# Kernel tuning notes

Hardware: AMD Instinct MI355X
Metric: run time of the kernel (lower is better)

Reference implementation:

```python
import jax, jax.numpy as jnp
import numpy as np

B = 16            # batch of graphs
N = 512           # n_node
D = 32            # embedding_dim
MAXN = 16         # max_neighbors
E = MAXN * (N - 1)   # 8176 edges per graph
SLEFT = N * D
FSS = 601         # full_support_size
NA = N - 1        # num_actions (so one-hot rows == B*n_node)
IN0 = D + 1       # sa feature dim
NTOT = B * N


def _gat(x, snd, rcv, W, a_src, a_dst, b):
    # single-head GATConv, add_self_loops=False
    h = x @ W                                            # [BN, C]
    e = (h * a_src).sum(-1)[snd] + (h * a_dst).sum(-1)[rcv]
    e = jnp.where(e > 0, e, 0.2 * e)                     # LeakyReLU(0.2)
    m = jax.ops.segment_max(e, rcv, num_segments=NTOT)   # segment softmax
    m = jnp.where(jnp.isfinite(m), m, 0.0)
    ee = jnp.exp(e - m[rcv])
    den = jax.ops.segment_sum(ee, rcv, num_segments=NTOT)
    alpha = ee / (den[rcv] + 1e-16)
    return jax.ops.segment_sum(alpha[:, None] * h[snd], rcv, num_segments=NTOT) + b


def _ln(x, s, o):
    # hk.LayerNorm(axis=-2): normalize over node axis, scale/offset over features
    x3 = x.reshape(B, N, -1)
    mu = x3.mean(axis=1, keepdims=True)
    var = ((x3 - mu) ** 2).mean(axis=1, keepdims=True)
    return ((x3 - mu) * jax.lax.rsqrt(var + 1e-5) * s + o).reshape(B * N, -1)


def _gat_params(key, din, dout):
    k1, k2, k3 = jax.random.split(key, 3)
    sc = 1.0 / np.sqrt(din)
    return (jax.random.normal(k1, (din, dout), jnp.float32) * sc,
            jax.random.normal(k2, (dout,), jnp.float32) * sc,
            jax.random.normal(k3, (dout,), jnp.float32) * sc,
            jnp.zeros((dout,), jnp.float32))


def setup_inputs():
    key = jax.random.key(0)
    ks = jax.random.split(key, 4)
    nodes = jax.random.normal(ks[0], (B, SLEFT), jnp.float32)
    snd = jax.random.randint(ks[1], (B, E), 0, N).astype(jnp.float32)
    rcv = jax.random.randint(ks[2], (B, E), 0, N).astype(jnp.float32)
    ns = jnp.concatenate([nodes, snd, rcv], axis=1)      # [B, SLEFT + 2E]
    a = jax.random.randint(ks[3], (B,), 0, NA + 1)
    inp = {"ns": ns, "a": a}
    dims = [(IN0, 4 * D), (4 * D, 2 * D), (2 * D, 2 * D), (2 * D, D)]
    rdims = [(IN0, FSS), (FSS, FSS), (FSS, FSS), (FSS, FSS)]
    for i, (di, do) in enumerate(dims, 1):
        W, asrc, adst, b = _gat_params(jax.random.fold_in(key, 100 + i), di, do)
        inp.update({f"W{i}": W, f"a{i}s": asrc, f"a{i}d": adst, f"b{i}": b})
        if i < 4:
            inp.update({f"s{i}": jnp.ones((do,), jnp.float32), f"o{i}": jnp.zeros((do,), jnp.float32)})
    for i, (di, do) in enumerate(rdims, 1):
        W, asrc, adst, b = _gat_params(jax.random.fold_in(key, 200 + i), di, do)
        inp.update({f"rW{i}": W, f"ra{i}s": asrc, f"ra{i}d": adst, f"rb{i}": b})
        if i < 4:
            inp.update({f"rs{i}": jnp.ones((FSS,), jnp.float32), f"ro{i}": jnp.zeros((FSS,), jnp.float32)})
    return inp


def reference(ns, a,
              W1, a1s, a1d, b1, s1, o1,
              W2, a2s, a2d, b2, s2, o2,
              W3, a3s, a3d, b3, s3, o3,
              W4, a4s, a4d, b4,
              rW1, ra1s, ra1d, rb1, rs1, ro1,
              rW2, ra2s, ra2d, rb2, rs2, ro2,
              rW3, ra3s, ra3d, rb3, rs3, ro3,
              rW4, ra4s, ra4d, rb4):
    # gbatch: offset per-graph indices into one big graph
    off = (jnp.arange(B, dtype=jnp.int32) * N)[:, None]
    snd = (ns[:, SLEFT:SLEFT + E].astype(jnp.int32) + off).reshape(-1)
    rcv = (ns[:, SLEFT + E:SLEFT + 2 * E].astype(jnp.int32) + off).reshape(-1)
    nodes = ns[:, :SLEFT].reshape(B * N, D)
    sa = jnp.concatenate([nodes, jax.nn.one_hot(a, NA + 1).reshape(-1, 1)], axis=1)
    # reward head
    r = jax.nn.relu(_ln(_gat(sa, snd, rcv, rW1, ra1s, ra1d, rb1), rs1, ro1))
    r = jax.nn.relu(_ln(_gat(r, snd, rcv, rW2, ra2s, ra2d, rb2), rs2, ro2))
    r = jax.nn.relu(_ln(_gat(r, snd, rcv, rW3, ra3s, ra3d, rb3), rs3, ro3))
    r = _gat(r, snd, rcv, rW4, ra4s, ra4d, rb4).reshape(B, N, FSS).sum(axis=1)
    # next-state head
    f = jax.nn.relu(_ln(_gat(sa, snd, rcv, W1, a1s, a1d, b1), s1, o1))
    f = jax.nn.relu(_ln(_gat(f, snd, rcv, W2, a2s, a2d, b2), s2, o2))
    f = jax.nn.relu(_ln(_gat(f, snd, rcv, W3, a3s, a3d, b3), s3, o3))
    f = _gat(f, snd, rcv, W4, a4s, a4d, b4).reshape(B, N * D)
    ns_new = jnp.concatenate([f, ns[:, SLEFT:]], axis=1)
    return (r, ns_new)
```

## Files before the change

### kernel.cpp

```cpp
#include <hip/hip_runtime.h>
#include <math.h>

#define B_ 16
#define N_ 512
#define D_ 32
#define E_ 8176
#define SLEFT_ 16384
#define FSS_ 601
#define BN_ (B_*N_)
#define BE_ (B_*E_)
#define NSROW_ (SLEFT_ + 2*E_)
#define OUT_R_ (B_*FSS_)
#define HLD_ 768

typedef __attribute__((ext_vector_type(8))) short short8;
typedef __attribute__((ext_vector_type(4))) float f32x4;

typedef __attribute__((address_space(3))) uint lds_uint;
typedef __attribute__((address_space(1))) const uint g_uint;

__device__ __forceinline__ void gl_lds16(const ushort* gp, ushort* lp) {
  __builtin_amdgcn_global_load_lds((g_uint*)gp, (lds_uint*)lp, 16, 0, 0);
}

__device__ __forceinline__ ushort f2b(float f) {
  uint u = __builtin_bit_cast(uint, f);
  u += 0x7FFFu + ((u >> 16) & 1u);
  return (ushort)(u >> 16);
}
__device__ __forceinline__ float b2f(ushort h) {
  return __builtin_bit_cast(float, ((uint)h) << 16);
}


__global__ __launch_bounds__(256) void k_indices(const float* __restrict__ ns,
                                                 int* __restrict__ src_i,
                                                 int* __restrict__ dst_i,
                                                 int* __restrict__ cnt) {
  int idx = blockIdx.x*256 + threadIdx.x;
  if (idx >= BE_) return;
  int b = idx / E_;
  int j = idx - b*E_;
  const float* row = ns + (size_t)b*NSROW_;
  int s = (int)row[SLEFT_ + j];
  int r = (int)row[SLEFT_ + E_ + j];
  src_i[idx] = b*N_ + s;
  int dst = b*N_ + r;
  dst_i[idx] = dst;
  atomicAdd(&cnt[dst], 1);
}

__global__ __launch_bounds__(1024) void k_scan(const int* __restrict__ cnt,
                                               int* __restrict__ rowptr) {
  __shared__ int part[1024];
  int t = threadIdx.x;
  int base = t*8;
  int loc[8]; int s = 0;
  #pragma unroll
  for (int i=0;i<8;i++){ loc[i]=cnt[base+i]; s+=loc[i]; }
  part[t]=s; __syncthreads();
  for (int off=1; off<1024; off<<=1) {
    int v = (t>=off)?part[t-off]:0;
    __syncthreads();
    part[t]+=v;
    __syncthreads();
  }
  int ex = (t==0)?0:part[t-1];
  #pragma unroll
  for (int i=0;i<8;i++){ rowptr[base+i]=ex; ex+=loc[i]; }
  if (t==1023) rowptr[BN_]=ex;
}

__global__ __launch_bounds__(256) void k_scatter(const int* __restrict__ src_i,
                                                 const int* __restrict__ dst_i,
                                                 const int* __restrict__ rowptr,
                                                 int* __restrict__ fill,
                                                 int* __restrict__ csr_src) {
  int idx = blockIdx.x*256+threadIdx.x;
  if (idx>=BE_) return;
  int dst = dst_i[idx];
  int pos = rowptr[dst] + atomicAdd(&fill[dst],1);
  csr_src[pos] = src_i[idx];
}


__global__ __launch_bounds__(256) void k_sa(const float* __restrict__ ns,
                                            const int* __restrict__ a,
                                            ushort* __restrict__ sa) {
  int idx = blockIdx.x*256+threadIdx.x;
  if (idx >= BN_*64) return;
  int v = idx >> 6, c = idx & 63;
  int b = v >> 9, n = v & 511;
  float val = 0.f;
  if (c < 32)       val = ns[(size_t)b*NSROW_ + n*32 + c];
  else if (c == 32) val = (a[b]==n) ? 1.f : 0.f;
  sa[idx] = f2b(val);
}


struct WtP { const float* Wr[4]; const float* Wn[4]; ushort* T[4]; };

__global__ __launch_bounds__(256) void k_wt_tr(WtP p) {
  int t = blockIdx.x;
  int s, base, KP, DINR, DINN, DOUTN, KOFF;
  if (t < 48)        { s=0; base=0;    KP=64;  DINR=33;  DINN=33;  DOUTN=128; KOFF=0;   }
  else if (t < 600)  { s=1; base=48;   KP=736; DINR=601; DINN=128; DOUTN=64;  KOFF=608; }
  else if (t < 1104) { s=2; base=600;  KP=672; DINR=601; DINN=64;  DOUTN=64;  KOFF=608; }
  else               { s=3; base=1104; KP=672; DINR=601; DINN=64;  DOUTN=32;  KOFF=608; }
  int ti = t - base;
  int kt = ti / 24, nt = ti - kt*24;
  int k0 = kt*32, n0 = nt*32;
  __shared__ float tile[32][33];
  int tid = threadIdx.x;
  int cc = tid & 31, rr = tid >> 5;
  #pragma unroll
  for (int it=0; it<4; it++) {
    int k = k0 + it*8 + rr;
    int n = n0 + cc;
    float v = 0.f;
    if (n < 640) { if (n < 601 && k < DINR) v = p.Wr[s][(size_t)k*601 + n]; }
    else { int nn = n-640, kk = k-KOFF;
           if (nn < DOUTN && kk >= 0 && kk < DINN) v = p.Wn[s][(size_t)kk*DOUTN + nn]; }
    tile[it*8+rr][cc] = v;
  }
  __syncthreads();
  #pragma unroll
  for (int it=0; it<4; it++) {
    int n = n0 + it*8 + rr;
    int k = k0 + cc;
    p.T[s][(size_t)n*KP + k] = f2b(tile[cc][it*8+rr]);
  }
}


__global__ __launch_bounds__(256) void k_gemm(const ushort* __restrict__ A,
                                              const ushort* __restrict__ Bt,
                                              ushort* __restrict__ C,
                                              float* __restrict__ esed,
                                              const float* __restrict__ asr,
                                              const float* __restrict__ adr,
                                              const float* __restrict__ asn,
                                              const float* __restrict__ adn,
                                              int Kpad, int dn) {
  __shared__ ushort Asm[64*32];
  __shared__ ushort Bsm[128*32];
  int tid = threadIdx.x;
  int rowBase = blockIdx.y * 64;
  int colBase = blockIdx.x * 128;
  int wave = tid >> 6, lane = tid & 63;
  int wr = (wave >> 1) * 32, wc = (wave & 1) * 64;
  int lm = lane & 15, lk = (lane >> 4) * 8;

  f32x4 acc[2][4];
  #pragma unroll
  for (int i=0;i<2;i++)
    #pragma unroll
    for (int j=0;j<4;j++) acc[i][j] = (f32x4){0.f,0.f,0.f,0.f};

  int t0 = tid, t1 = tid + 256;
  const ushort* Ag0 = A  + (size_t)(rowBase + (t0>>2))*Kpad + (t0&3)*8;
  const ushort* Bg0 = Bt + (size_t)(colBase + (t0>>2))*Kpad + (t0&3)*8;
  const ushort* Bg1 = Bt + (size_t)(colBase + (t1>>2))*Kpad + (t1&3)*8;
  ushort* Al0 = &Asm[t0*8];
  ushort* Bl0 = &Bsm[t0*8];
  ushort* Bl1 = &Bsm[t1*8];

  for (int k0 = 0; k0 < Kpad; k0 += 32) {
    gl_lds16(Ag0 + k0, Al0);
    gl_lds16(Bg0 + k0, Bl0);
    gl_lds16(Bg1 + k0, Bl1);
    __syncthreads();
    short8 af[2], bfr[4];
    #pragma unroll
    for (int i=0;i<2;i++) af[i]  = *(short8*)&Asm[(wr + i*16 + lm)*32 + lk];
    #pragma unroll
    for (int j=0;j<4;j++) bfr[j] = *(short8*)&Bsm[(wc + j*16 + lm)*32 + lk];
    #pragma unroll
    for (int i=0;i<2;i++)
      #pragma unroll
      for (int j=0;j<4;j++)
        acc[i][j] = __builtin_amdgcn_mfma_f32_16x16x32_bf16(af[i], bfr[j], acc[i][j], 0,0,0);
    __syncthreads();
  }

  float asv[4], adv[4];
  #pragma unroll
  for (int j=0;j<4;j++) {
    int col = colBase + wc + j*16 + lm;
    float s = 0.f, d = 0.f;
    if (col < 601)      { s = asr[col];     d = adr[col]; }
    else if (col >= 640 && col - 640 < dn) { s = asn[col-640]; d = adn[col-640]; }
    asv[j] = s; adv[j] = d;
  }
  int cr = lane >> 4;
  int ct2 = blockIdx.x*2 + (wc >> 6);
  #pragma unroll
  for (int i=0;i<2;i++) {
    #pragma unroll
    for (int j=0;j<4;j++) {
      int col = colBase + wc + j*16 + lm;
      #pragma unroll
      for (int g=0; g<4; g++) {
        int row = rowBase + wr + i*16 + cr*4 + g;
        C[(size_t)row*HLD_ + col] = f2b(acc[i][j][g]);
      }
    }
    #pragma unroll
    for (int g=0; g<4; g++) {
      float se = 0.f, sd = 0.f;
      #pragma unroll
      for (int j=0;j<4;j++) { se += acc[i][j][g]*asv[j]; sd += acc[i][j][g]*adv[j]; }
      #pragma unroll
      for (int o=1;o<16;o<<=1) { se += __shfl_xor(se,o,64); sd += __shfl_xor(sd,o,64); }
      if (lm == 0) {
        int row = rowBase + wr + i*16 + cr*4 + g;
        esed[(size_t)row*24 + ct2*2 + 0] = se;
        esed[(size_t)row*24 + ct2*2 + 1] = sd;
      }
    }
  }
}


__global__ __launch_bounds__(256) void k_agg(const ushort* __restrict__ h,
                                             const float* __restrict__ esed,
                                             const int* __restrict__ rowptr,
                                             const int* __restrict__ csr,
                                             const float* __restrict__ bias_r,
                                             const float* __restrict__ bias_n,
                                             ushort* __restrict__ g,
                                             int dn) {
  int wid = threadIdx.x>>6, lane = threadIdx.x&63;
  int bid = blockIdx.x;
  int xcd = bid & 7, slot = bid >> 3;
  int graph = xcd + ((slot >> 7) << 3);
  int v = graph*512 + (slot & 127)*4 + wid;
  int s0 = rowptr[v], e0 = rowptr[v+1];
  int deg = e0 - s0;

  float edr = 0.f, edn = 0.f;
  {
    const float* ep = esed + (size_t)v*24;
    #pragma unroll
    for (int t=0;t<10;t++) edr += ep[2*t+1];
    edn = ep[21] + ep[23];
  }

  int ch0 = lane, ch1 = lane + 64;
  bool a1 = ch1 < 96;
  float acc0[8], acc1[8];
  #pragma unroll
  for (int q=0;q<8;q++){ acc0[q]=0.f; acc1[q]=0.f; }

  if (deg <= 64) {
    bool has = lane < deg;
    int u = 0; float er = -__builtin_inff(), en = -__builtin_inff();
    if (has) {
      u = csr[s0 + lane];
      const float* ep = esed + (size_t)u*24;
      float sr = 0.f;
      #pragma unroll
      for (int t=0;t<10;t++) sr += ep[2*t];
      float sn = ep[20] + ep[22];
      er = sr + edr; er = er > 0.f ? er : 0.2f*er;
      en = sn + edn; en = en > 0.f ? en : 0.2f*en;
    }
    float mr = er, mn = en;
    #pragma unroll
    for (int o=32;o;o>>=1) { mr = fmaxf(mr, __shfl_xor(mr,o,64)); mn = fmaxf(mn, __shfl_xor(mn,o,64)); }
    float pr = has ? __expf(er - mr) : 0.f;
    float pn = has ? __expf(en - mn) : 0.f;
    float dr = pr, dnm = pn;
    #pragma unroll
    for (int o=32;o;o>>=1) { dr += __shfl_xor(dr,o,64); dnm += __shfl_xor(dnm,o,64); }
    pr *= 1.f/(dr + 1e-16f);
    pn *= 1.f/(dnm + 1e-16f);

    short8 A0{}, Bv0{}, A1{}, Bv1{};
    float w0r=0.f, w0n=0.f, w1r=0.f, w1n=0.f;
    if (deg > 0) {
      w0r = __shfl(pr, 0, 64); w0n = __shfl(pn, 0, 64); int uu = __shfl(u, 0, 64);
      const ushort* hp = h + (size_t)uu*HLD_;
      A0 = *(const short8*)&hp[ch0*8];
      if (a1) Bv0 = *(const short8*)&hp[ch1*8];
    }
    if (deg > 1) {
      w1r = __shfl(pr, 1, 64); w1n = __shfl(pn, 1, 64); int uu = __shfl(u, 1, 64);
      const ushort* hp = h + (size_t)uu*HLD_;
      A1 = *(const short8*)&hp[ch0*8];
      if (a1) Bv1 = *(const short8*)&hp[ch1*8];
    }
    bool c1r = ch1 < 80;
    for (int t = 0; t < deg; ++t) {
      short8 A2{}, Bv2{}; float w2r=0.f, w2n=0.f;
      if (t+2 < deg) {
        w2r = __shfl(pr, t+2, 64); w2n = __shfl(pn, t+2, 64); int uu = __shfl(u, t+2, 64);
        const ushort* hp = h + (size_t)uu*HLD_;
        A2 = *(const short8*)&hp[ch0*8];
        if (a1) Bv2 = *(const short8*)&hp[ch1*8];
      }
      #pragma unroll
      for (int q=0;q<8;q++) acc0[q] += w0r * b2f((ushort)A0[q]);
      if (a1) {
        float w = c1r ? w0r : w0n;
        #pragma unroll
        for (int q=0;q<8;q++) acc1[q] += w * b2f((ushort)Bv0[q]);
      }
      A0=A1; Bv0=Bv1; w0r=w1r; w0n=w1n;
      A1=A2; Bv1=Bv2; w1r=w2r; w1n=w2n;
    }
  } else {
    float mr = -__builtin_inff(), mn = -__builtin_inff();
    for (int j = s0 + lane; j < e0; j += 64) {
      const float* ep = esed + (size_t)csr[j]*24;
      float sr=0.f; for (int t=0;t<10;t++) sr += ep[2*t];
      float sn = ep[20]+ep[22];
      float er = sr + edr; er = er>0.f?er:0.2f*er;
      float en = sn + edn; en = en>0.f?en:0.2f*en;
      mr = fmaxf(mr, er); mn = fmaxf(mn, en);
    }
    #pragma unroll
    for (int o=32;o;o>>=1) { mr=fmaxf(mr,__shfl_xor(mr,o,64)); mn=fmaxf(mn,__shfl_xor(mn,o,64)); }
    float dr=0.f, dnm=0.f;
    for (int j = s0 + lane; j < e0; j += 64) {
      const float* ep = esed + (size_t)csr[j]*24;
      float sr=0.f; for (int t=0;t<10;t++) sr += ep[2*t];
      float sn = ep[20]+ep[22];
      float er = sr + edr; er = er>0.f?er:0.2f*er;
      float en = sn + edn; en = en>0.f?en:0.2f*en;
      dr += __expf(er-mr); dnm += __expf(en-mn);
    }
    #pragma unroll
    for (int o=32;o;o>>=1) { dr+=__shfl_xor(dr,o,64); dnm+=__shfl_xor(dnm,o,64); }
    float ir = 1.f/(dr+1e-16f), in_ = 1.f/(dnm+1e-16f);
    bool c1r = ch1 < 80;
    for (int j = s0; j < e0; ++j) {
      int uu = csr[j];
      const float* ep = esed + (size_t)uu*24;
      float sr=0.f; for (int t=0;t<10;t++) sr += ep[2*t];
      float sn = ep[20]+ep[22];
      float er = sr + edr; er = er>0.f?er:0.2f*er;
      float en = sn + edn; en = en>0.f?en:0.2f*en;
      float wr2 = __expf(er-mr)*ir, wn2 = __expf(en-mn)*in_;
      const ushort* hp = h + (size_t)uu*HLD_;
      short8 hv = *(const short8*)&hp[ch0*8];
      #pragma unroll
      for (int q=0;q<8;q++) acc0[q] += wr2 * b2f((ushort)hv[q]);
      if (a1) {
        short8 hv2 = *(const short8*)&hp[ch1*8];
        float w = c1r ? wr2 : wn2;
        #pragma unroll
        for (int q=0;q<8;q++) acc1[q] += w * b2f((ushort)hv2[q]);
      }
    }
  }

  ushort* gv = g + (size_t)v*HLD_;
  {
    int cb = ch0*8;
    short8 ov;
    #pragma unroll
    for (int q=0;q<8;q++) ov[q] = (short)f2b(acc0[q] + bias_r[cb+q]);
    *(short8*)&gv[cb] = ov;
  }
  if (a1) {
    int cb = ch1*8;
    short8 ov;
    #pragma unroll
    for (int q=0;q<8;q++) {
      int c = cb+q;
      float val;
      if (c < 601)                         val = acc1[q] + bias_r[c];
      else if (c >= 640 && (c-640) < dn)   val = acc1[q] + bias_n[c-640];
      else                                 val = 0.f;
      ov[q] = (short)f2b(val);
    }
    *(short8*)&gv[cb] = ov;
  }
}


__global__ __launch_bounds__(256) void k_ln_stats(const ushort* __restrict__ g,
                                                  float* __restrict__ st) {
  int b = blockIdx.y, z = blockIdx.z; int n0 = z*64;
  int lc = threadIdx.x & 63, r0 = threadIdx.x >> 6;
  int c = blockIdx.x*64 + lc;
  float s=0.f, q=0.f;
  #pragma unroll 4
  for (int i=0;i<16;i++) {
    int n = n0 + r0*16 + i;
    float x = b2f(g[(size_t)(b*N_+n)*HLD_ + c]);
    s+=x; q+=x*x;
  }
  __shared__ float S[4][64], Q[4][64];
  S[r0][lc]=s; Q[r0][lc]=q; __syncthreads();
  if (r0==0) {
    st[((size_t)(z*2+0)*B_ + b)*HLD_ + c] = S[0][lc]+S[1][lc]+S[2][lc]+S[3][lc];
    st[((size_t)(z*2+1)*B_ + b)*HLD_ + c] = Q[0][lc]+Q[1][lc]+Q[2][lc]+Q[3][lc];
  }
}


__global__ __launch_bounds__(256) void k_ln_apply(const ushort* __restrict__ g,
                                                  const float* __restrict__ st,
                                                  const float* __restrict__ scr,
                                                  const float* __restrict__ ofr,
                                                  const float* __restrict__ scn,
                                                  const float* __restrict__ ofn,
                                                  ushort* __restrict__ xb,
                                                  int dn, int Kpad) {
  int tid = threadIdx.x;
  int pp = blockIdx.x*128 + (tid & 127);
  int c0 = pp*2;
  if (c0 >= Kpad) return;
  int vbase = blockIdx.y*16;
  int b = vbase >> 9;
  float mv[2], av[2];
  #pragma unroll
  for (int q=0;q<2;q++) {
    int c = c0+q;
    int cs; bool valid; float scale, offs;
    if (c < 608) { cs = c; valid = c < 601;
                   scale = valid ? scr[c] : 0.f; offs = valid ? ofr[c] : 0.f; }
    else { int cn = c - 608; cs = 640 + cn; valid = cn < dn;
           scale = valid ? scn[cn] : 0.f; offs = valid ? ofn[cn] : 0.f; }
    float mul = 0.f, add = 0.f;
    if (valid) {
      float s=0.f, qq=0.f;
      #pragma unroll
      for (int z=0;z<8;z++) {
        s  += st[((size_t)(z*2+0)*B_ + b)*HLD_ + cs];
        qq += st[((size_t)(z*2+1)*B_ + b)*HLD_ + cs];
      }
      float mu = s*(1.f/N_);
      float var = qq*(1.f/N_) - mu*mu;
      float rs = rsqrtf(var+1e-5f);
      mul = rs*scale;
      add = offs - mu*rs*scale;
    }
    mv[q] = mul; av[q] = add;
  }
  int cs0 = (c0 < 608) ? c0 : 640 + (c0 - 608);
  for (int i = tid >> 7; i < 16; i += 2) {
    int v = vbase + i;
    uint gg = *(const uint*)&g[(size_t)v*HLD_ + cs0];
    float x0 = b2f((ushort)(gg & 0xFFFFu));
    float x1 = b2f((ushort)(gg >> 16));
    float y0 = x0*mv[0] + av[0]; y0 = y0 > 0.f ? y0 : 0.f;
    float y1 = x1*mv[1] + av[1]; y1 = y1 > 0.f ? y1 : 0.f;
    *(uint*)&xb[(size_t)v*Kpad + c0] = ((uint)f2b(y1) << 16) | f2b(y0);
  }
}


__global__ __launch_bounds__(256) void k_rsum(const ushort* __restrict__ g,
                                              float* __restrict__ rsp) {
  int b = blockIdx.y, z = blockIdx.z; int n0 = z*64;
  int lc = threadIdx.x & 63, r0 = threadIdx.x>>6;
  int c = blockIdx.x*64 + lc;
  float s = 0.f;
  if (c < FSS_) {
    #pragma unroll 4
    for (int i=0;i<16;i++) {
      int n = n0 + r0*16 + i;
      s += b2f(g[(size_t)(b*N_+n)*HLD_ + c]);
    }
  }
  __shared__ float S[4][64];
  S[r0][lc]=s; __syncthreads();
  if (r0==0 && c<FSS_)
    rsp[((size_t)z*B_ + b)*FSS_ + c] = S[0][lc]+S[1][lc]+S[2][lc]+S[3][lc];
}


__global__ __launch_bounds__(256) void k_final(const float* __restrict__ rsp,
                                               const ushort* __restrict__ g,
                                               const float* __restrict__ ns,
                                               float* __restrict__ out) {
  int idx = blockIdx.x*256+threadIdx.x;
  if (idx < OUT_R_) {
    int b = idx / FSS_, c = idx - b*FSS_;
    float s = 0.f;
    #pragma unroll
    for (int z=0;z<8;z++) s += rsp[((size_t)z*B_ + b)*FSS_ + c];
    out[idx] = s;
  } else {
    int j2 = idx - OUT_R_;
    if (j2 >= B_*NSROW_) return;
    int b = j2 / NSROW_; int j = j2 - b*NSROW_;
    float v;
    if (j < SLEFT_) {
      int n = j >> 5, c = j & 31;
      v = b2f(g[(size_t)(b*N_+n)*HLD_ + 640 + c]);
    } else {
      v = ns[(size_t)b*NSROW_ + j];
    }
    out[idx] = v;
  }
}


extern "C" void kernel_launch(void* const* d_in, const int* in_sizes, int n_in,
                              void* d_out, int out_size, void* d_ws, size_t ws_size,
                              hipStream_t stream) {
  const float* ns = (const float*)d_in[0];
  const int*   a  = (const int*)d_in[1];

  const float *W[4], *As[4], *Ad[4], *Bb[4], *Sc[3], *Of[3];
  const float *rW[4], *rAs[4], *rAd[4], *rBb[4], *rSc[3], *rOf[3];
  int p = 2;
  for (int i=0;i<4;i++){
    W[i]=(const float*)d_in[p++]; As[i]=(const float*)d_in[p++];
    Ad[i]=(const float*)d_in[p++]; Bb[i]=(const float*)d_in[p++];
    if (i<3){ Sc[i]=(const float*)d_in[p++]; Of[i]=(const float*)d_in[p++]; }
  }
  for (int i=0;i<4;i++){
    rW[i]=(const float*)d_in[p++]; rAs[i]=(const float*)d_in[p++];
    rAd[i]=(const float*)d_in[p++]; rBb[i]=(const float*)d_in[p++];
    if (i<3){ rSc[i]=(const float*)d_in[p++]; rOf[i]=(const float*)d_in[p++]; }
  }

  char* w = (char*)d_ws;
  auto carve = [&](size_t bytes)->void* {
    void* r = (void*)w;
    w += (bytes + 255) & ~(size_t)255;
    return r;
  };
  ushort* xb   = (ushort*)carve((size_t)BN_*736*2);
  ushort* hbuf = (ushort*)carve((size_t)BN_*HLD_*2);
  ushort* gbuf = (ushort*)carve((size_t)BN_*HLD_*2);
  ushort* sabf = (ushort*)carve((size_t)BN_*64*2);
  float* esed  = (float*)carve((size_t)BN_*24*4);
  float* stp   = (float*)carve((size_t)16*B_*HLD_*4);
  float* rsp   = (float*)carve((size_t)8*B_*FSS_*4);
  int* src_i   = (int*)carve((size_t)BE_*4);
  int* dst_i   = (int*)carve((size_t)BE_*4);
  int* cnt     = (int*)carve((size_t)2*BN_*4);
  int* fill    = cnt + BN_;
  int* rowptr  = (int*)carve((size_t)(BN_+1)*4);
  int* csr_src = (int*)carve((size_t)BE_*4);
  ushort* Wt[4];
  Wt[0] = (ushort*)carve((size_t)768*64*2);
  Wt[1] = (ushort*)carve((size_t)768*736*2);
  Wt[2] = (ushort*)carve((size_t)768*672*2);
  Wt[3] = (ushort*)carve((size_t)768*672*2);

  float* out = (float*)d_out;

  hipMemsetAsync(cnt, 0, (size_t)2*BN_*4, stream);

  k_indices<<<(BE_+255)/256, 256, 0, stream>>>(ns, src_i, dst_i, cnt);
  k_scan<<<1, 1024, 0, stream>>>(cnt, rowptr);
  k_scatter<<<(BE_+255)/256, 256, 0, stream>>>(src_i, dst_i, rowptr, fill, csr_src);
  k_sa<<<(BN_*64+255)/256, 256, 0, stream>>>(ns, a, sabf);

  WtP wtp;
  for (int i=0;i<4;i++){ wtp.Wr[i]=rW[i]; wtp.Wn[i]=W[i]; wtp.T[i]=Wt[i]; }
  k_wt_tr<<<1608, 256, 0, stream>>>(wtp);

  dim3 ggrid(6, BN_/64);

  k_gemm<<<ggrid, 256, 0, stream>>>(sabf, Wt[0], hbuf, esed, rAs[0],rAd[0],As[0],Ad[0], 64, 128);
  k_agg<<<BN_/4, 256, 0, stream>>>(hbuf, esed, rowptr, csr_src, rBb[0], Bb[0], gbuf, 128);
  k_ln_stats<<<dim3(12, B_, 8), 256, 0, stream>>>(gbuf, stp);
  k_ln_apply<<<dim3(3, BN_/16), 256, 0, stream>>>(gbuf, stp, rSc[0],rOf[0],Sc[0],Of[0], xb, 128, 736);

  k_gemm<<<ggrid, 256, 0, stream>>>(xb, Wt[1], hbuf, esed, rAs[1],rAd[1],As[1],Ad[1], 736, 64);
  k_agg<<<BN_/4, 256, 0, stream>>>(hbuf, esed, rowptr, csr_src, rBb[1], Bb[1], gbuf, 64);
  k_ln_stats<<<dim3(12, B_, 8), 256, 0, stream>>>(gbuf, stp);
  k_ln_apply<<<dim3(3, BN_/16), 256, 0, stream>>>(gbuf, stp, rSc[1],rOf[1],Sc[1],Of[1], xb, 64, 672);

  k_gemm<<<ggrid, 256, 0, stream>>>(xb, Wt[2], hbuf, esed, rAs[2],rAd[2],As[2],Ad[2], 672, 64);
  k_agg<<<BN_/4, 256, 0, stream>>>(hbuf, esed, rowptr, csr_src, rBb[2], Bb[2], gbuf, 64);
  k_ln_stats<<<dim3(12, B_, 8), 256, 0, stream>>>(gbuf, stp);
  k_ln_apply<<<dim3(3, BN_/16), 256, 0, stream>>>(gbuf, stp, rSc[2],rOf[2],Sc[2],Of[2], xb, 64, 672);

  k_gemm<<<ggrid, 256, 0, stream>>>(xb, Wt[3], hbuf, esed, rAs[3],rAd[3],As[3],Ad[3], 672, 32);
  k_agg<<<BN_/4, 256, 0, stream>>>(hbuf, esed, rowptr, csr_src, rBb[3], Bb[3], gbuf, 32);

  k_rsum<<<dim3(10, B_, 8), 256, 0, stream>>>(gbuf, rsp);
  k_final<<<(OUT_R_ + B_*NSROW_ + 255)/256, 256, 0, stream>>>(rsp, gbuf, ns, out);
}
```

Before: 409.6 us.

## Split GAT aggregation into edge-weight pass and LDS-tiled per-graph aggregation with fused stats

The GEMM epilogue now reduces attention logits into four compact per-node arrays with atomics, replacing the 24-wide partial layout. A new k_ew kernel computes normalized softmax edge weights once per edge. A new k_aggt kernel stages a graph's 64-column slice of h in LDS and aggregates from there, and it also computes the per-graph column sums and sums of squares. This removes the separate LayerNorm-stats and reward-sum kernels. The trade-offs are only 192 blocks with a serial 128-node loop per wave, a 64 KB LDS footprint, scalar per-column LDS reads, atomic contention, and an extra memset per layer.

```diff
diff --git a/kernel.cpp b/kernel.cpp
--- a/kernel.cpp
+++ b/kernel.cpp
@@ -194,6 +194,7 @@
   }
   int cr = lane >> 4;
   int ct2 = blockIdx.x*2 + (wc >> 6);
+  float* esp = (ct2 < 10) ? esed : esed + 2*BN_;
   #pragma unroll
   for (int i=0;i<2;i++) {
     #pragma unroll
@@ -214,189 +215,154 @@
       for (int o=1;o<16;o<<=1) { se += __shfl_xor(se,o,64); sd += __shfl_xor(sd,o,64); }
       if (lm == 0) {
         int row = rowBase + wr + i*16 + cr*4 + g;
-        esed[(size_t)row*24 + ct2*2 + 0] = se;
-        esed[(size_t)row*24 + ct2*2 + 1] = sd;
+        atomicAdd(&esp[row], se);
+        atomicAdd(&esp[BN_ + row], sd);
       }
     }
   }
 }
 
 
-__global__ __launch_bounds__(256) void k_agg(const ushort* __restrict__ h,
-                                             const float* __restrict__ esed,
-                                             const int* __restrict__ rowptr,
-                                             const int* __restrict__ csr,
-                                             const float* __restrict__ bias_r,
-                                             const float* __restrict__ bias_n,
-                                             ushort* __restrict__ g,
-                                             int dn) {
+__global__ __launch_bounds__(256) void k_ew(const float* __restrict__ esed,
+                                            const int* __restrict__ rowptr,
+                                            const int* __restrict__ csr,
+                                            float* __restrict__ wrv,
+                                            float* __restrict__ wnv) {
+  const float* es_r = esed;
+  const float* ed_r = esed + BN_;
+  const float* es_n = esed + 2*BN_;
+  const float* ed_n = esed + 3*BN_;
   int wid = threadIdx.x>>6, lane = threadIdx.x&63;
-  int bid = blockIdx.x;
-  int xcd = bid & 7, slot = bid >> 3;
-  int graph = xcd + ((slot >> 7) << 3);
-  int v = graph*512 + (slot & 127)*4 + wid;
+  int v = blockIdx.x*4 + wid;
   int s0 = rowptr[v], e0 = rowptr[v+1];
   int deg = e0 - s0;
-
-  float edr = 0.f, edn = 0.f;
-  {
-    const float* ep = esed + (size_t)v*24;
-    #pragma unroll
-    for (int t=0;t<10;t++) edr += ep[2*t+1];
-    edn = ep[21] + ep[23];
-  }
-
-  int ch0 = lane, ch1 = lane + 64;
-  bool a1 = ch1 < 96;
-  float acc0[8], acc1[8];
-  #pragma unroll
-  for (int q=0;q<8;q++){ acc0[q]=0.f; acc1[q]=0.f; }
+  if (deg == 0) return;
+  float edr = ed_r[v], edn = ed_n[v];
 
   if (deg <= 64) {
     bool has = lane < deg;
-    int u = 0; float er = -__builtin_inff(), en = -__builtin_inff();
+    float er = -__builtin_inff(), en = -__builtin_inff();
     if (has) {
-      u = csr[s0 + lane];
-      const float* ep = esed + (size_t)u*24;
-      float sr = 0.f;
-      #pragma unroll
-      for (int t=0;t<10;t++) sr += ep[2*t];
-      float sn = ep[20] + ep[22];
-      er = sr + edr; er = er > 0.f ? er : 0.2f*er;
-      en = sn + edn; en = en > 0.f ? en : 0.2f*en;
+      int u = csr[s0 + lane];
+      er = es_r[u] + edr; er = er > 0.f ? er : 0.2f*er;
+      en = es_n[u] + edn; en = en > 0.f ? en : 0.2f*en;
     }
     float mr = er, mn = en;
     #pragma unroll
     for (int o=32;o;o>>=1) { mr = fmaxf(mr, __shfl_xor(mr,o,64)); mn = fmaxf(mn, __shfl_xor(mn,o,64)); }
     float pr = has ? __expf(er - mr) : 0.f;
     float pn = has ? __expf(en - mn) : 0.f;
-    float dr = pr, dnm = pn;
-    #pragma unroll
-    for (int o=32;o;o>>=1) { dr += __shfl_xor(dr,o,64); dnm += __shfl_xor(dnm,o,64); }
-    pr *= 1.f/(dr + 1e-16f);
-    pn *= 1.f/(dnm + 1e-16f);
-
-    short8 A0{}, Bv0{}, A1{}, Bv1{};
-    float w0r=0.f, w0n=0.f, w1r=0.f, w1n=0.f;
-    if (deg > 0) {
-      w0r = __shfl(pr, 0, 64); w0n = __shfl(pn, 0, 64); int uu = __shfl(u, 0, 64);
-      const ushort* hp = h + (size_t)uu*HLD_;
-      A0 = *(const short8*)&hp[ch0*8];
-      if (a1) Bv0 = *(const short8*)&hp[ch1*8];
-    }
-    if (deg > 1) {
-      w1r = __shfl(pr, 1, 64); w1n = __shfl(pn, 1, 64); int uu = __shfl(u, 1, 64);
-      const ushort* hp = h + (size_t)uu*HLD_;
-      A1 = *(const short8*)&hp[ch0*8];
-      if (a1) Bv1 = *(const short8*)&hp[ch1*8];
-    }
-    bool c1r = ch1 < 80;
-    for (int t = 0; t < deg; ++t) {
-      short8 A2{}, Bv2{}; float w2r=0.f, w2n=0.f;
-      if (t+2 < deg) {
-        w2r = __shfl(pr, t+2, 64); w2n = __shfl(pn, t+2, 64); int uu = __shfl(u, t+2, 64);
-        const ushort* hp = h + (size_t)uu*HLD_;
-        A2 = *(const short8*)&hp[ch0*8];
-        if (a1) Bv2 = *(const short8*)&hp[ch1*8];
-      }
-      #pragma unroll
-      for (int q=0;q<8;q++) acc0[q] += w0r * b2f((ushort)A0[q]);
-      if (a1) {
-        float w = c1r ? w0r : w0n;
-        #pragma unroll
-        for (int q=0;q<8;q++) acc1[q] += w * b2f((ushort)Bv0[q]);
-      }
-      A0=A1; Bv0=Bv1; w0r=w1r; w0n=w1n;
-      A1=A2; Bv1=Bv2; w1r=w2r; w1n=w2n;
+    float dr = pr, dn2 = pn;
+    #pragma unroll
+    for (int o=32;o;o>>=1) { dr += __shfl_xor(dr,o,64); dn2 += __shfl_xor(dn2,o,64); }
+    if (has) {
+      wrv[s0 + lane] = pr * (1.f/(dr + 1e-16f));
+      wnv[s0 + lane] = pn * (1.f/(dn2 + 1e-16f));
     }
   } else {
     float mr = -__builtin_inff(), mn = -__builtin_inff();
     for (int j = s0 + lane; j < e0; j += 64) {
-      const float* ep = esed + (size_t)csr[j]*24;
-      float sr=0.f; for (int t=0;t<10;t++) sr += ep[2*t];
-      float sn = ep[20]+ep[22];
-      float er = sr + edr; er = er>0.f?er:0.2f*er;
-      float en = sn + edn; en = en>0.f?en:0.2f*en;
+      int u = csr[j];
+      float er = es_r[u] + edr; er = er>0.f?er:0.2f*er;
+      float en = es_n[u] + edn; en = en>0.f?en:0.2f*en;
       mr = fmaxf(mr, er); mn = fmaxf(mn, en);
     }
     #pragma unroll
     for (int o=32;o;o>>=1) { mr=fmaxf(mr,__shfl_xor(mr,o,64)); mn=fmaxf(mn,__shfl_xor(mn,o,64)); }
-    float dr=0.f, dnm=0.f;
+    float dr=0.f, dn2=0.f;
     for (int j = s0 + lane; j < e0; j += 64) {
-      const float* ep = esed + (size_t)csr[j]*24;
-      float sr=0.f; for (int t=0;t<10;t++) sr += ep[2*t];
-      float sn = ep[20]+ep[22];
-      float er = sr + edr; er = er>0.f?er:0.2f*er;
-      float en = sn + edn; en = en>0.f?en:0.2f*en;
-      dr += __expf(er-mr); dnm += __expf(en-mn);
-    }
-    #pragma unroll
-    for (int o=32;o;o>>=1) { dr+=__shfl_xor(dr,o,64); dnm+=__shfl_xor(dnm,o,64); }
-    float ir = 1.f/(dr+1e-16f), in_ = 1.f/(dnm+1e-16f);
-    bool c1r = ch1 < 80;
-    for (int j = s0; j < e0; ++j) {
-      int uu = csr[j];
-      const float* ep = esed + (size_t)uu*24;
-      float sr=0.f; for (int t=0;t<10;t++) sr += ep[2*t];
-      float sn = ep[20]+ep[22];
-      float er = sr + edr; er = er>0.f?er:0.2f*er;
-      float en = sn + edn; en = en>0.f?en:0.2f*en;
-      float wr2 = __expf(er-mr)*ir, wn2 = __expf(en-mn)*in_;
-      const ushort* hp = h + (size_t)uu*HLD_;
-      short8 hv = *(const short8*)&hp[ch0*8];
-      #pragma unroll
-      for (int q=0;q<8;q++) acc0[q] += wr2 * b2f((ushort)hv[q]);
-      if (a1) {
-        short8 hv2 = *(const short8*)&hp[ch1*8];
-        float w = c1r ? wr2 : wn2;
-        #pragma unroll
-        for (int q=0;q<8;q++) acc1[q] += w * b2f((ushort)hv2[q]);
+      int u = csr[j];
+      float er = es_r[u] + edr; er = er>0.f?er:0.2f*er;
+      float en = es_n[u] + edn; en = en>0.f?en:0.2f*en;
+      dr += __expf(er-mr); dn2 += __expf(en-mn);
+    }
+    #pragma unroll
+    for (int o=32;o;o>>=1) { dr+=__shfl_xor(dr,o,64); dn2+=__shfl_xor(dn2,o,64); }
+    float ir = 1.f/(dr+1e-16f), in_ = 1.f/(dn2+1e-16f);
+    for (int j = s0 + lane; j < e0; j += 64) {
+      int u = csr[j];
+      float er = es_r[u] + edr; er = er>0.f?er:0.2f*er;
+      float en = es_n[u] + edn; en = en>0.f?en:0.2f*en;
+      wrv[j] = __expf(er-mr)*ir;
+      wnv[j] = __expf(en-mn)*in_;
+    }
+  }
+}
+
+
+__global__ __launch_bounds__(256) void k_aggt(const ushort* __restrict__ h,
+                                              const float* __restrict__ wrv,
+                                              const float* __restrict__ wnv,
+                                              const int* __restrict__ rowptr,
+                                              const int* __restrict__ csr,
+                                              const float* __restrict__ bias_r,
+                                              const float* __restrict__ bias_n,
+                                              ushort* __restrict__ g,
+                                              float* __restrict__ st,
+                                              int dn) {
+  __shared__ ushort Hl[512*64];
+  int bid = blockIdx.x;
+  int graph = bid & 15;
+  int chunk = bid >> 4;
+  int c0 = chunk * 64;
+  const float* wv = (chunk < 10) ? wrv : wnv;
+  int lane = threadIdx.x & 63, wid = threadIdx.x >> 6;
+
+  {
+    int t = threadIdx.x;
+    int col8 = (t & 7) * 8;
+    int rb = t >> 3;
+    #pragma unroll
+    for (int i = 0; i < 16; i++) {
+      int r = i*32 + rb;
+      *(short8*)&Hl[r*64 + col8] =
+        *(const short8*)&h[(size_t)(graph*512 + r)*HLD_ + c0 + col8];
+    }
+  }
+  __syncthreads();
+
+  int col = c0 + lane;
+  bool valid; float bv;
+  if (col < 601)                         { bv = bias_r[col];     valid = true; }
+  else if (col >= 640 && col - 640 < dn) { bv = bias_n[col-640]; valid = true; }
+  else                                   { bv = 0.f;             valid = false; }
+
+  float ssum = 0.f, sq = 0.f;
+  for (int i = 0; i < 128; i++) {
+    int vn = graph*512 + wid*128 + i;
+    int s0 = rowptr[vn], e0 = rowptr[vn+1];
+    float acc = 0.f;
+    for (int base = s0; base < e0; base += 64) {
+      int j = base + lane;
+      float wj = 0.f; int uj = 0;
+      if (j < e0) { wj = wv[j]; uj = csr[j] & 511; }
+      int cl = e0 - base; if (cl > 64) cl = 64;
+      float wb0 = __shfl(wj, 0, 64); int ub0 = __shfl(uj, 0, 64);
+      ushort hv0 = Hl[ub0*64 + lane];
+      for (int t = 0; t < cl; ++t) {
+        float wb1 = 0.f; int ub1 = 0; ushort hv1 = 0;
+        if (t+1 < cl) {
+          wb1 = __shfl(wj, t+1, 64); ub1 = __shfl(uj, t+1, 64);
+          hv1 = Hl[ub1*64 + lane];
+        }
+        acc += wb0 * b2f(hv0);
+        wb0 = wb1; hv0 = hv1;
       }
     }
-  }
-
-  ushort* gv = g + (size_t)v*HLD_;
-  {
-    int cb = ch0*8;
-    short8 ov;
-    #pragma unroll
-    for (int q=0;q<8;q++) ov[q] = (short)f2b(acc0[q] + bias_r[cb+q]);
-    *(short8*)&gv[cb] = ov;
-  }
-  if (a1) {
-    int cb = ch1*8;
-    short8 ov;
-    #pragma unroll
-    for (int q=0;q<8;q++) {
-      int c = cb+q;
-      float val;
-      if (c < 601)                         val = acc1[q] + bias_r[c];
-      else if (c >= 640 && (c-640) < dn)   val = acc1[q] + bias_n[c-640];
-      else                                 val = 0.f;
-      ov[q] = (short)f2b(val);
-    }
-    *(short8*)&gv[cb] = ov;
-  }
-}
-
-
-__global__ __launch_bounds__(256) void k_ln_stats(const ushort* __restrict__ g,
-                                                  float* __restrict__ st) {
-  int b = blockIdx.y, z = blockIdx.z; int n0 = z*64;
-  int lc = threadIdx.x & 63, r0 = threadIdx.x >> 6;
-  int c = blockIdx.x*64 + lc;
-  float s=0.f, q=0.f;
-  #pragma unroll 4
-  for (int i=0;i<16;i++) {
-    int n = n0 + r0*16 + i;
-    float x = b2f(g[(size_t)(b*N_+n)*HLD_ + c]);
-    s+=x; q+=x*x;
-  }
-  __shared__ float S[4][64], Q[4][64];
-  S[r0][lc]=s; Q[r0][lc]=q; __syncthreads();
-  if (r0==0) {
-    st[((size_t)(z*2+0)*B_ + b)*HLD_ + c] = S[0][lc]+S[1][lc]+S[2][lc]+S[3][lc];
-    st[((size_t)(z*2+1)*B_ + b)*HLD_ + c] = Q[0][lc]+Q[1][lc]+Q[2][lc]+Q[3][lc];
+    float val = valid ? acc + bv : 0.f;
+    g[(size_t)vn*HLD_ + col] = f2b(val);
+    ssum += val; sq += val*val;
+  }
+  __syncthreads();
+  float* Sf = (float*)Hl;
+  Sf[wid*64 + lane]       = ssum;
+  Sf[256 + wid*64 + lane] = sq;
+  __syncthreads();
+  if (wid == 0) {
+    float s = Sf[lane] + Sf[64+lane] + Sf[128+lane] + Sf[192+lane];
+    float q = Sf[256+lane] + Sf[320+lane] + Sf[384+lane] + Sf[448+lane];
+    st[(size_t)graph*HLD_ + col]        = s;
+    st[(size_t)(B_+graph)*HLD_ + col]   = q;
   }
 }
 
@@ -426,12 +392,8 @@
            scale = valid ? scn[cn] : 0.f; offs = valid ? ofn[cn] : 0.f; }
     float mul = 0.f, add = 0.f;
     if (valid) {
-      float s=0.f, qq=0.f;
-      #pragma unroll
-      for (int z=0;z<8;z++) {
-        s  += st[((size_t)(z*2+0)*B_ + b)*HLD_ + cs];
-        qq += st[((size_t)(z*2+1)*B_ + b)*HLD_ + cs];
-      }
+      float s  = st[(size_t)b*HLD_ + cs];
+      float qq = st[(size_t)(B_+b)*HLD_ + cs];
       float mu = s*(1.f/N_);
       float var = qq*(1.f/N_) - mu*mu;
       float rs = rsqrtf(var+1e-5f);
@@ -453,37 +415,14 @@
 }
 
 
-__global__ __launch_bounds__(256) void k_rsum(const ushort* __restrict__ g,
-                                              float* __restrict__ rsp) {
-  int b = blockIdx.y, z = blockIdx.z; int n0 = z*64;
-  int lc = threadIdx.x & 63, r0 = threadIdx.x>>6;
-  int c = blockIdx.x*64 + lc;
-  float s = 0.f;
-  if (c < FSS_) {
-    #pragma unroll 4
-    for (int i=0;i<16;i++) {
-      int n = n0 + r0*16 + i;
-      s += b2f(g[(size_t)(b*N_+n)*HLD_ + c]);
-    }
-  }
-  __shared__ float S[4][64];
-  S[r0][lc]=s; __syncthreads();
-  if (r0==0 && c<FSS_)
-    rsp[((size_t)z*B_ + b)*FSS_ + c] = S[0][lc]+S[1][lc]+S[2][lc]+S[3][lc];
-}
-
-
-__global__ __launch_bounds__(256) void k_final(const float* __restrict__ rsp,
+__global__ __launch_bounds__(256) void k_final(const float* __restrict__ st,
                                                const ushort* __restrict__ g,
                                                const float* __restrict__ ns,
                                                float* __restrict__ out) {
   int idx = blockIdx.x*256+threadIdx.x;
   if (idx < OUT_R_) {
     int b = idx / FSS_, c = idx - b*FSS_;
-    float s = 0.f;
-    #pragma unroll
-    for (int z=0;z<8;z++) s += rsp[((size_t)z*B_ + b)*FSS_ + c];
-    out[idx] = s;
+    out[idx] = st[(size_t)b*HLD_ + c];
   } else {
     int j2 = idx - OUT_R_;
     if (j2 >= B_*NSROW_) return;
@@ -530,9 +469,10 @@
   ushort* hbuf = (ushort*)carve((size_t)BN_*HLD_*2);
   ushort* gbuf = (ushort*)carve((size_t)BN_*HLD_*2);
   ushort* sabf = (ushort*)carve((size_t)BN_*64*2);
-  float* esed  = (float*)carve((size_t)BN_*24*4);
-  float* stp   = (float*)carve((size_t)16*B_*HLD_*4);
-  float* rsp   = (float*)carve((size_t)8*B_*FSS_*4);
+  float* esed  = (float*)carve((size_t)4*BN_*4);
+  float* wrv   = (float*)carve((size_t)BE_*4);
+  float* wnv   = (float*)carve((size_t)BE_*4);
+  float* st    = (float*)carve((size_t)2*B_*HLD_*4);
   int* src_i   = (int*)carve((size_t)BE_*4);
   int* dst_i   = (int*)carve((size_t)BE_*4);
   int* cnt     = (int*)carve((size_t)2*BN_*4);
@@ -560,24 +500,23 @@
 
   dim3 ggrid(6, BN_/64);
 
-  k_gemm<<<ggrid, 256, 0, stream>>>(sabf, Wt[0], hbuf, esed, rAs[0],rAd[0],As[0],Ad[0], 64, 128);
-  k_agg<<<BN_/4, 256, 0, stream>>>(hbuf, esed, rowptr, csr_src, rBb[0], Bb[0], gbuf, 128);
-  k_ln_stats<<<dim3(12, B_, 8), 256, 0, stream>>>(gbuf, stp);
-  k_ln_apply<<<dim3(3, BN_/16), 256, 0, stream>>>(gbuf, stp, rSc[0],rOf[0],Sc[0],Of[0], xb, 128, 736);
-
-  k_gemm<<<ggrid, 256, 0, stream>>>(xb, Wt[1], hbuf, esed, rAs[1],rAd[1],As[1],Ad[1], 736, 64);
-  k_agg<<<BN_/4, 256, 0, stream>>>(hbuf, esed, rowptr, csr_src, rBb[1], Bb[1], gbuf, 64);
-  k_ln_stats<<<dim3(12, B_, 8), 256, 0, stream>>>(gbuf, stp);
-  k_ln_apply<<<dim3(3, BN_/16), 256, 0, stream>>>(gbuf, stp, rSc[1],rOf[1],Sc[1],Of[1], xb, 64, 672);
-
-  k_gemm<<<ggrid, 256, 0, stream>>>(xb, Wt[2], hbuf, esed, rAs[2],rAd[2],As[2],Ad[2], 672, 64);
-  k_agg<<<BN_/4, 256, 0, stream>>>(hbuf, esed, rowptr, csr_src, rBb[2], Bb[2], gbuf, 64);
-  k_ln_stats<<<dim3(12, B_, 8), 256, 0, stream>>>(gbuf, stp);
-  k_ln_apply<<<dim3(3, BN_/16), 256, 0, stream>>>(gbuf, stp, rSc[2],rOf[2],Sc[2],Of[2], xb, 64, 672);
-
-  k_gemm<<<ggrid, 256, 0, stream>>>(xb, Wt[3], hbuf, esed, rAs[3],rAd[3],As[3],Ad[3], 672, 32);
-  k_agg<<<BN_/4, 256, 0, stream>>>(hbuf, esed, rowptr, csr_src, rBb[3], Bb[3], gbuf, 32);
-
-  k_rsum<<<dim3(10, B_, 8), 256, 0, stream>>>(gbuf, rsp);
-  k_final<<<(OUT_R_ + B_*NSROW_ + 255)/256, 256, 0, stream>>>(rsp, gbuf, ns, out);
-}
+  const ushort* xin[4] = { sabf, xb, xb, xb };
+  int Kp[4]  = { 64, 736, 672, 672 };
+  int dns[4] = { 128, 64, 64, 32 };
+
+  for (int L=0; L<4; ++L) {
+    hipMemsetAsync(esed, 0, (size_t)4*BN_*4, stream);
+    k_gemm<<<ggrid, 256, 0, stream>>>(xin[L], Wt[L], hbuf, esed,
+                                      rAs[L], rAd[L], As[L], Ad[L], Kp[L], dns[L]);
+    k_ew<<<BN_/4, 256, 0, stream>>>(esed, rowptr, csr_src, wrv, wnv);
+    k_aggt<<<192, 256, 0, stream>>>(hbuf, wrv, wnv, rowptr, csr_src,
+                                    rBb[L], Bb[L], gbuf, st, dns[L]);
+    if (L < 3) {
+      int Kpn = (L==0) ? 736 : 672;
+      k_ln_apply<<<dim3(3, BN_/16), 256, 0, stream>>>(gbuf, st,
+                  rSc[L], rOf[L], Sc[L], Of[L], xb, dns[L], Kpn);
+    }
+  }
+
+  k_final<<<(OUT_R_ + B_*NSROW_ + 255)/256, 256, 0, stream>>>(st, gbuf, ns, out);
+}
```

Result: slower. 1.400 ms (+241.9%).

## Reduce attention logits with atomics into compact arrays and batch neighbor gathers

Applied to the files above, without the earlier changes.

The GEMM epilogue now atomically accumulates per-node source and destination attention scores into four compact BN-length arrays, replacing the 24-float partial-sum row per node. This lets the aggregation kernel read one float per neighbor instead of summing twelve strided partials, at the cost of a memset before each layer and float atomics whose summation order is nondeterministic. The neighbor gather loop is also changed from a two-deep software-pipelined prefetch to batches of four loads issued before the accumulation, and the layer launches are folded into a loop.

```diff
diff --git a/kernel.cpp b/kernel.cpp
--- a/kernel.cpp
+++ b/kernel.cpp
@@ -194,6 +194,7 @@
   }
   int cr = lane >> 4;
   int ct2 = blockIdx.x*2 + (wc >> 6);
+  float* esp = (ct2 < 10) ? esed : esed + 2*BN_;
   #pragma unroll
   for (int i=0;i<2;i++) {
     #pragma unroll
@@ -214,8 +215,8 @@
       for (int o=1;o<16;o<<=1) { se += __shfl_xor(se,o,64); sd += __shfl_xor(sd,o,64); }
       if (lm == 0) {
         int row = rowBase + wr + i*16 + cr*4 + g;
-        esed[(size_t)row*24 + ct2*2 + 0] = se;
-        esed[(size_t)row*24 + ct2*2 + 1] = sd;
+        atomicAdd(&esp[row], se);
+        atomicAdd(&esp[BN_ + row], sd);
       }
     }
   }
@@ -230,6 +231,10 @@
                                              const float* __restrict__ bias_n,
                                              ushort* __restrict__ g,
                                              int dn) {
+  const float* es_r = esed;
+  const float* ed_r = esed + BN_;
+  const float* es_n = esed + 2*BN_;
+  const float* ed_n = esed + 3*BN_;
   int wid = threadIdx.x>>6, lane = threadIdx.x&63;
   int bid = blockIdx.x;
   int xcd = bid & 7, slot = bid >> 3;
@@ -237,17 +242,11 @@
   int v = graph*512 + (slot & 127)*4 + wid;
   int s0 = rowptr[v], e0 = rowptr[v+1];
   int deg = e0 - s0;
-
-  float edr = 0.f, edn = 0.f;
-  {
-    const float* ep = esed + (size_t)v*24;
-    #pragma unroll
-    for (int t=0;t<10;t++) edr += ep[2*t+1];
-    edn = ep[21] + ep[23];
-  }
+  float edr = ed_r[v], edn = ed_n[v];
 
   int ch0 = lane, ch1 = lane + 64;
   bool a1 = ch1 < 96;
+  bool c1r = ch1 < 80;
   float acc0[8], acc1[8];
   #pragma unroll
   for (int q=0;q<8;q++){ acc0[q]=0.f; acc1[q]=0.f; }
@@ -257,13 +256,8 @@
     int u = 0; float er = -__builtin_inff(), en = -__builtin_inff();
     if (has) {
       u = csr[s0 + lane];
-      const float* ep = esed + (size_t)u*24;
-      float sr = 0.f;
-      #pragma unroll
-      for (int t=0;t<10;t++) sr += ep[2*t];
-      float sn = ep[20] + ep[22];
-      er = sr + edr; er = er > 0.f ? er : 0.2f*er;
-      en = sn + edn; en = en > 0.f ? en : 0.2f*en;
+      er = es_r[u] + edr; er = er > 0.f ? er : 0.2f*er;
+      en = es_n[u] + edn; en = en > 0.f ? en : 0.2f*en;
     }
     float mr = er, mn = en;
     #pragma unroll
@@ -276,71 +270,58 @@
     pr *= 1.f/(dr + 1e-16f);
     pn *= 1.f/(dnm + 1e-16f);
 
-    short8 A0{}, Bv0{}, A1{}, Bv1{};
-    float w0r=0.f, w0n=0.f, w1r=0.f, w1n=0.f;
-    if (deg > 0) {
-      w0r = __shfl(pr, 0, 64); w0n = __shfl(pn, 0, 64); int uu = __shfl(u, 0, 64);
-      const ushort* hp = h + (size_t)uu*HLD_;
-      A0 = *(const short8*)&hp[ch0*8];
-      if (a1) Bv0 = *(const short8*)&hp[ch1*8];
-    }
-    if (deg > 1) {
-      w1r = __shfl(pr, 1, 64); w1n = __shfl(pn, 1, 64); int uu = __shfl(u, 1, 64);
-      const ushort* hp = h + (size_t)uu*HLD_;
-      A1 = *(const short8*)&hp[ch0*8];
-      if (a1) Bv1 = *(const short8*)&hp[ch1*8];
-    }
-    bool c1r = ch1 < 80;
-    for (int t = 0; t < deg; ++t) {
-      short8 A2{}, Bv2{}; float w2r=0.f, w2n=0.f;
-      if (t+2 < deg) {
-        w2r = __shfl(pr, t+2, 64); w2n = __shfl(pn, t+2, 64); int uu = __shfl(u, t+2, 64);
-        const ushort* hp = h + (size_t)uu*HLD_;
-        A2 = *(const short8*)&hp[ch0*8];
-        if (a1) Bv2 = *(const short8*)&hp[ch1*8];
+    for (int t0 = 0; t0 < deg; t0 += 4) {
+      int nt = deg - t0; if (nt > 4) nt = 4;
+      short8 va[4], vb[4];
+      float w0[4], w1[4];
+      #pragma unroll
+      for (int q=0;q<4;q++) {
+        if (q < nt) {
+          int uu = __shfl(u, t0+q, 64);
+          w0[q] = __shfl(pr, t0+q, 64);
+          w1[q] = __shfl(pn, t0+q, 64);
+          const ushort* hp = h + (size_t)uu*HLD_;
+          va[q] = *(const short8*)&hp[ch0*8];
+          vb[q] = a1 ? *(const short8*)&hp[ch1*8] : short8{};
+        } else {
+          w0[q] = 0.f; w1[q] = 0.f; va[q] = short8{}; vb[q] = short8{};
+        }
       }
       #pragma unroll
-      for (int q=0;q<8;q++) acc0[q] += w0r * b2f((ushort)A0[q]);
-      if (a1) {
-        float w = c1r ? w0r : w0n;
+      for (int q=0;q<4;q++) {
         #pragma unroll
-        for (int q=0;q<8;q++) acc1[q] += w * b2f((ushort)Bv0[q]);
+        for (int r=0;r<8;r++) acc0[r] += w0[q] * b2f((ushort)va[q][r]);
+        if (a1) {
+          float wv = c1r ? w0[q] : w1[q];
+          #pragma unroll
+          for (int r=0;r<8;r++) acc1[r] += wv * b2f((ushort)vb[q][r]);
+        }
       }
-      A0=A1; Bv0=Bv1; w0r=w1r; w0n=w1n;
-      A1=A2; Bv1=Bv2; w1r=w2r; w1n=w2n;
     }
   } else {
     float mr = -__builtin_inff(), mn = -__builtin_inff();
     for (int j = s0 + lane; j < e0; j += 64) {
-      const float* ep = esed + (size_t)csr[j]*24;
-      float sr=0.f; for (int t=0;t<10;t++) sr += ep[2*t];
-      float sn = ep[20]+ep[22];
-      float er = sr + edr; er = er>0.f?er:0.2f*er;
-      float en = sn + edn; en = en>0.f?en:0.2f*en;
+      int u = csr[j];
+      float er = es_r[u] + edr; er = er>0.f?er:0.2f*er;
+      float en = es_n[u] + edn; en = en>0.f?en:0.2f*en;
       mr = fmaxf(mr, er); mn = fmaxf(mn, en);
     }
     #pragma unroll
     for (int o=32;o;o>>=1) { mr=fmaxf(mr,__shfl_xor(mr,o,64)); mn=fmaxf(mn,__shfl_xor(mn,o,64)); }
     float dr=0.f, dnm=0.f;
     for (int j = s0 + lane; j < e0; j += 64) {
-      const float* ep = esed + (size_t)csr[j]*24;
-      float sr=0.f; for (int t=0;t<10;t++) sr += ep[2*t];
-      float sn = ep[20]+ep[22];
-      float er = sr + edr; er = er>0.f?er:0.2f*er;
-      float en = sn + edn; en = en>0.f?en:0.2f*en;
+      int u = csr[j];
+      float er = es_r[u] + edr; er = er>0.f?er:0.2f*er;
+      float en = es_n[u] + edn; en = en>0.f?en:0.2f*en;
       dr += __expf(er-mr); dnm += __expf(en-mn);
     }
     #pragma unroll
     for (int o=32;o;o>>=1) { dr+=__shfl_xor(dr,o,64); dnm+=__shfl_xor(dnm,o,64); }
     float ir = 1.f/(dr+1e-16f), in_ = 1.f/(dnm+1e-16f);
-    bool c1r = ch1 < 80;
     for (int j = s0; j < e0; ++j) {
       int uu = csr[j];
-      const float* ep = esed + (size_t)uu*24;
-      float sr=0.f; for (int t=0;t<10;t++) sr += ep[2*t];
-      float sn = ep[20]+ep[22];
-      float er = sr + edr; er = er>0.f?er:0.2f*er;
-      float en = sn + edn; en = en>0.f?en:0.2f*en;
+      float er = es_r[uu] + edr; er = er>0.f?er:0.2f*er;
+      float en = es_n[uu] + edn; en = en>0.f?en:0.2f*en;
       float wr2 = __expf(er-mr)*ir, wn2 = __expf(en-mn)*in_;
       const ushort* hp = h + (size_t)uu*HLD_;
       short8 hv = *(const short8*)&hp[ch0*8];
@@ -348,9 +329,9 @@
       for (int q=0;q<8;q++) acc0[q] += wr2 * b2f((ushort)hv[q]);
       if (a1) {
         short8 hv2 = *(const short8*)&hp[ch1*8];
-        float w = c1r ? wr2 : wn2;
+        float wv = c1r ? wr2 : wn2;
         #pragma unroll
-        for (int q=0;q<8;q++) acc1[q] += w * b2f((ushort)hv2[q]);
+        for (int q=0;q<8;q++) acc1[q] += wv * b2f((ushort)hv2[q]);
       }
     }
   }
@@ -530,7 +511,7 @@
   ushort* hbuf = (ushort*)carve((size_t)BN_*HLD_*2);
   ushort* gbuf = (ushort*)carve((size_t)BN_*HLD_*2);
   ushort* sabf = (ushort*)carve((size_t)BN_*64*2);
-  float* esed  = (float*)carve((size_t)BN_*24*4);
+  float* esed  = (float*)carve((size_t)4*BN_*4);
   float* stp   = (float*)carve((size_t)16*B_*HLD_*4);
   float* rsp   = (float*)carve((size_t)8*B_*FSS_*4);
   int* src_i   = (int*)carve((size_t)BE_*4);
@@ -560,23 +541,23 @@
 
   dim3 ggrid(6, BN_/64);
 
-  k_gemm<<<ggrid, 256, 0, stream>>>(sabf, Wt[0], hbuf, esed, rAs[0],rAd[0],As[0],Ad[0], 64, 128);
-  k_agg<<<BN_/4, 256, 0, stream>>>(hbuf, esed, rowptr, csr_src, rBb[0], Bb[0], gbuf, 128);
-  k_ln_stats<<<dim3(12, B_, 8), 256, 0, stream>>>(gbuf, stp);
-  k_ln_apply<<<dim3(3, BN_/16), 256, 0, stream>>>(gbuf, stp, rSc[0],rOf[0],Sc[0],Of[0], xb, 128, 736);
-
-  k_gemm<<<ggrid, 256, 0, stream>>>(xb, Wt[1], hbuf, esed, rAs[1],rAd[1],As[1],Ad[1], 736, 64);
-  k_agg<<<BN_/4, 256, 0, stream>>>(hbuf, esed, rowptr, csr_src, rBb[1], Bb[1], gbuf, 64);
-  k_ln_stats<<<dim3(12, B_, 8), 256, 0, stream>>>(gbuf, stp);
-  k_ln_apply<<<dim3(3, BN_/16), 256, 0, stream>>>(gbuf, stp, rSc[1],rOf[1],Sc[1],Of[1], xb, 64, 672);
-
-  k_gemm<<<ggrid, 256, 0, stream>>>(xb, Wt[2], hbuf, esed, rAs[2],rAd[2],As[2],Ad[2], 672, 64);
-  k_agg<<<BN_/4, 256, 0, stream>>>(hbuf, esed, rowptr, csr_src, rBb[2], Bb[2], gbuf, 64);
-  k_ln_stats<<<dim3(12, B_, 8), 256, 0, stream>>>(gbuf, stp);
-  k_ln_apply<<<dim3(3, BN_/16), 256, 0, stream>>>(gbuf, stp, rSc[2],rOf[2],Sc[2],Of[2], xb, 64, 672);
-
-  k_gemm<<<ggrid, 256, 0, stream>>>(xb, Wt[3], hbuf, esed, rAs[3],rAd[3],As[3],Ad[3], 672, 32);
-  k_agg<<<BN_/4, 256, 0, stream>>>(hbuf, esed, rowptr, csr_src, rBb[3], Bb[3], gbuf, 32);
+  const ushort* xin[4] = { sabf, xb, xb, xb };
+  int Kp[4]  = { 64, 736, 672, 672 };
+  int dns[4] = { 128, 64, 64, 32 };
+
+  for (int L=0; L<4; ++L) {
+    hipMemsetAsync(esed, 0, (size_t)4*BN_*4, stream);
+    k_gemm<<<ggrid, 256, 0, stream>>>(xin[L], Wt[L], hbuf, esed,
+                                      rAs[L], rAd[L], As[L], Ad[L], Kp[L], dns[L]);
+    k_agg<<<BN_/4, 256, 0, stream>>>(hbuf, esed, rowptr, csr_src,
+                                     rBb[L], Bb[L], gbuf, dns[L]);
+    if (L < 3) {
+      k_ln_stats<<<dim3(12, B_, 8), 256, 0, stream>>>(gbuf, stp);
+      int Kpn = (L==0) ? 736 : 672;
+      k_ln_apply<<<dim3(3, BN_/16), 256, 0, stream>>>(gbuf, stp,
+                  rSc[L], rOf[L], Sc[L], Of[L], xb, dns[L], Kpn);
+    }
+  }
 
   k_rsum<<<dim3(10, B_, 8), 256, 0, stream>>>(gbuf, rsp);
   k_final<<<(OUT_R_ + B_*NSROW_ + 255)/256, 256, 0, stream>>>(rsp, gbuf, ns, out);
```

Measured after the change: 397.1 us. 3.0% less time.
